# Optimization experiments

Measured on AMD Instinct MI355X. Metric: run time of the kernel, lower is better.

Reference implementation:

```python
import jax, jax.numpy as jnp
import numpy as np

B, T, I, H = 64, 512, 1024, 1024


def setup_inputs() -> dict:
    key = jax.random.key(0)
    k1, k2, k3, k4 = jax.random.split(key, 4)
    scale_ih = (6.0 / (H + I)) ** 0.5  # xavier_uniform bound
    scale_hh = (6.0 / (H + H)) ** 0.5
    return {
        "x": jax.random.normal(k1, (B, T, I), dtype=jnp.float32),
        "h0": jax.random.normal(k2, (1, B, H), dtype=jnp.float32),
        "W_ih": jax.random.uniform(k3, (H, I), dtype=jnp.float32, minval=-scale_ih, maxval=scale_ih),
        "b_ih": jnp.zeros((H,), dtype=jnp.float32),
        "W_hh": jax.random.uniform(k4, (H, H), dtype=jnp.float32, minval=-scale_hh, maxval=scale_hh),
        "b_hh": jnp.zeros((H,), dtype=jnp.float32),
    }


def reference(x, h0, W_ih, b_ih, W_hh, b_hh):
    # h_t = tanh(x_t @ W_ih^T + b_ih + h_{t-1} @ W_hh^T + b_hh)
    # Precompute the input projection for all timesteps (same math, batched GEMM).
    xp = jnp.einsum("bti,hi->tbh", x, W_ih) + b_ih  # [T,B,H]
    h = h0[0]  # [B,H]

    def step(h, xp_t):
        h_new = jnp.tanh(xp_t + h @ W_hh.T + b_hh)
        return h_new, h_new

    _, ys = jax.lax.scan(step, h, xp)  # ys: [T,B,H]
    return jnp.transpose(ys, (1, 0, 2))  # [B,T,H]
```

## Files before the change

kernel.cpp:

```cpp
#include <hip/hip_runtime.h>
#include <hip/hip_bf16.h>

#define BB_   64
#define TT_   512
#define II_   1024
#define HH_   1024

typedef _Float16 half8  __attribute__((ext_vector_type(8)));
typedef _Float16 half4v __attribute__((ext_vector_type(4)));
typedef float    f32x4  __attribute__((ext_vector_type(4)));

__device__ __forceinline__ float fast_tanh(float x) {
    float t = fminf(fmaxf(x, -16.f), 16.f);
    float e = __builtin_amdgcn_exp2f(t * 2.885390082f);
    return 1.f - 2.f * __builtin_amdgcn_rcpf(e + 1.f);
}

__global__ __launch_bounds__(256) void gemm_xp(const float* __restrict__ x,
                                               const float* __restrict__ Wih,
                                               const float* __restrict__ bih,
                                               float* __restrict__ out) {
    __shared__ alignas(16) _Float16 As[128 * 40];
    __shared__ alignas(16) _Float16 Bs[128 * 40];

    const int tid  = threadIdx.x;
    const int bm   = blockIdx.x >> 3;
    const int bn   = blockIdx.x & 7;
    const int M0   = bm * 128, N0 = bn * 128;
    const int lane = tid & 63, w = tid >> 6;
    const int wm   = (w & 1) * 64, wn = (w >> 1) * 64;
    const int ro   = lane & 15, q = lane >> 4;
    const int sr   = tid >> 3, sc = tid & 7;

    const f32x4 zero4 = {0.f, 0.f, 0.f, 0.f};
    f32x4 acc[4][4];
    #pragma unroll
    for (int i = 0; i < 4; ++i)
        #pragma unroll
        for (int j = 0; j < 4; ++j) acc[i][j] = zero4;

    for (int kk = 0; kk < 32; ++kk) {
        const int k0 = kk * 32;
        #pragma unroll
        for (int ir = 0; ir < 4; ++ir) {
            const int row = ir * 32 + sr;
            const float4 av = *(const float4*)(x   + (size_t)(M0 + row) * II_ + k0 + sc * 4);
            const float4 bv = *(const float4*)(Wih + (size_t)(N0 + row) * II_ + k0 + sc * 4);
            half4v ah = { (_Float16)av.x, (_Float16)av.y, (_Float16)av.z, (_Float16)av.w };
            half4v bh = { (_Float16)bv.x, (_Float16)bv.y, (_Float16)bv.z, (_Float16)bv.w };
            *(half4v*)(As + row * 40 + sc * 4) = ah;
            *(half4v*)(Bs + row * 40 + sc * 4) = bh;
        }
        __syncthreads();

        half8 a[4], b[4];
        #pragma unroll
        for (int i = 0; i < 4; ++i) {
            a[i] = *(const half8*)(As + (wm + i * 16 + ro) * 40 + q * 8);
            b[i] = *(const half8*)(Bs + (wn + i * 16 + ro) * 40 + q * 8);
        }
        #pragma unroll
        for (int i = 0; i < 4; ++i)
            #pragma unroll
            for (int j = 0; j < 4; ++j)
                acc[i][j] = __builtin_amdgcn_mfma_f32_16x16x32_f16(a[i], b[j], acc[i][j], 0, 0, 0);
        __syncthreads();
    }

    #pragma unroll
    for (int j = 0; j < 4; ++j) {
        const int col = N0 + wn + j * 16 + ro;
        const float bias = bih[col];
        #pragma unroll
        for (int i = 0; i < 4; ++i) {
            #pragma unroll
            for (int r = 0; r < 4; ++r) {
                const int rowg = M0 + wm + i * 16 + q * 4 + r;
                out[(size_t)rowg * HH_ + col] = acc[i][j][r] + bias;
            }
        }
    }
}

__global__ __launch_bounds__(256, 1) void rnn_steps(const float* __restrict__ Whh,
                                                    const float* __restrict__ bhh,
                                                    const float* __restrict__ h0,
                                                    float* __restrict__ out,
                                                    unsigned* __restrict__ comm) {
    __shared__ alignas(16) _Float16 hbuf[2][5][1032];

    const int tid  = threadIdx.x;
    const int lane = tid & 63;
    const int w    = tid >> 6;
    const int g    = blockIdx.x >> 4;
    const int wg   = blockIdx.x & 15;
    const int b0   = g * 4;
    const int j0   = wg * 64;
    const int ro   = lane & 15, q = lane >> 4;
    const int arow = (ro < 4) ? ro : 4;
    const int bat  = lane >> 4;
    const int colw = j0 + w * 16 + (lane & 15);

    half8 wf[4][8];
    {
        const float* wrow = Whh + (size_t)(j0 + w * 16 + ro) * HH_;
        #pragma unroll
        for (int kq = 0; kq < 4; ++kq) {
            #pragma unroll
            for (int ks = 0; ks < 8; ++ks) {
                const int kc = kq * 256 + ks * 32 + q * 8;
                const float4 w0 = *(const float4*)(wrow + kc);
                const float4 w1 = *(const float4*)(wrow + kc + 4);
                half8 hv;
                hv[0] = (_Float16)w0.x; hv[1] = (_Float16)w0.y;
                hv[2] = (_Float16)w0.z; hv[3] = (_Float16)w0.w;
                hv[4] = (_Float16)w1.x; hv[5] = (_Float16)w1.y;
                hv[6] = (_Float16)w1.z; hv[7] = (_Float16)w1.w;
                wf[kq][ks] = hv;
            }
        }
    }
    const float bhh_r = bhh[colw];

    for (int i = tid; i < 1032; i += 256) {
        hbuf[0][4][i] = (_Float16)0.f;
        hbuf[1][4][i] = (_Float16)0.f;
    }

    const f32x4 zero4 = {0.f, 0.f, 0.f, 0.f};

    #define TAGOK_(v) ((((unsigned)((v) >> 16) & 0xffffu) == su) & \
                       ((unsigned)((v) >> 48) == su))

    for (int s = 0; s < TT_; ++s) {
        const int slot = s & 1;

        const float xpv = out[((size_t)(b0 + bat) * TT_ + s) * HH_ + colw];

        unsigned* dstw = (unsigned*)(&hbuf[slot][w][0]);
        if (s == 0) {
            const float2* hrow = (const float2*)(h0 + (size_t)(b0 + w) * HH_);
            #pragma unroll
            for (int c = 0; c < 8; ++c) {
                const float2 hv = hrow[c * 64 + lane];
                union { _Float16 h[2]; unsigned u; } pk;
                pk.h[0] = (_Float16)hv.x; pk.h[1] = (_Float16)hv.y;
                dstw[c * 64 + lane] = pk.u;
            }
        } else {
            const unsigned su = (unsigned)s;
            const unsigned long long* sp = (const unsigned long long*)
                (comm + (size_t)slot * (BB_ * HH_) + (size_t)(b0 + w) * HH_);
            unsigned long long v0, v1, v2, v3, v4, v5, v6, v7;
            bool ok = false;
            while (!ok) {
                v0 = __hip_atomic_load(sp + 0 * 64 + lane, __ATOMIC_RELAXED, __HIP_MEMORY_SCOPE_AGENT);
                v1 = __hip_atomic_load(sp + 1 * 64 + lane, __ATOMIC_RELAXED, __HIP_MEMORY_SCOPE_AGENT);
                v2 = __hip_atomic_load(sp + 2 * 64 + lane, __ATOMIC_RELAXED, __HIP_MEMORY_SCOPE_AGENT);
                v3 = __hip_atomic_load(sp + 3 * 64 + lane, __ATOMIC_RELAXED, __HIP_MEMORY_SCOPE_AGENT);
                v4 = __hip_atomic_load(sp + 4 * 64 + lane, __ATOMIC_RELAXED, __HIP_MEMORY_SCOPE_AGENT);
                v5 = __hip_atomic_load(sp + 5 * 64 + lane, __ATOMIC_RELAXED, __HIP_MEMORY_SCOPE_AGENT);
                v6 = __hip_atomic_load(sp + 6 * 64 + lane, __ATOMIC_RELAXED, __HIP_MEMORY_SCOPE_AGENT);
                v7 = __hip_atomic_load(sp + 7 * 64 + lane, __ATOMIC_RELAXED, __HIP_MEMORY_SCOPE_AGENT);
                bool o = true;
                o &= TAGOK_(v0); o &= TAGOK_(v1); o &= TAGOK_(v2); o &= TAGOK_(v3);
                o &= TAGOK_(v4); o &= TAGOK_(v5); o &= TAGOK_(v6); o &= TAGOK_(v7);
                ok = o;
            }
            #define PACK_(x) ((unsigned)((x) & 0xffffull) | (((unsigned)((x) >> 32)) << 16))
            dstw[0 * 64 + lane] = PACK_(v0);
            dstw[1 * 64 + lane] = PACK_(v1);
            dstw[2 * 64 + lane] = PACK_(v2);
            dstw[3 * 64 + lane] = PACK_(v3);
            dstw[4 * 64 + lane] = PACK_(v4);
            dstw[5 * 64 + lane] = PACK_(v5);
            dstw[6 * 64 + lane] = PACK_(v6);
            dstw[7 * 64 + lane] = PACK_(v7);
            #undef PACK_
        }
        __syncthreads();

        f32x4 acc[4] = {zero4, zero4, zero4, zero4};
        const _Float16* abase = &hbuf[slot][0][0] + (size_t)arow * 1032;
        #pragma unroll
        for (int kq = 0; kq < 4; ++kq) {
            #pragma unroll
            for (int ks = 0; ks < 8; ++ks) {
                const half8 a = *(const half8*)(abase + kq * 256 + ks * 32 + q * 8);
                acc[kq] = __builtin_amdgcn_mfma_f32_16x16x32_f16(a, wf[kq][ks], acc[kq], 0, 0, 0);
            }
        }

        const f32x4 sum = acc[0] + acc[1] + acc[2] + acc[3];
        const float t0 = __shfl(sum[0], lane & 15);
        const float t1 = __shfl(sum[1], lane & 15);
        const float t2 = __shfl(sum[2], lane & 15);
        const float t3 = __shfl(sum[3], lane & 15);
        const float val = (bat == 0) ? t0 : (bat == 1) ? t1 : (bat == 2) ? t2 : t3;

        const float hnew = fast_tanh(xpv + bhh_r + val);

        union { _Float16 h; unsigned short us; } cv; cv.h = (_Float16)hnew;
        const unsigned word = ((unsigned)(s + 1) << 16) | (unsigned)cv.us;
        __hip_atomic_store(comm + (size_t)((s + 1) & 1) * (BB_ * HH_)
                                + (size_t)(b0 + bat) * HH_ + colw,
                           word, __ATOMIC_RELAXED, __HIP_MEMORY_SCOPE_AGENT);

        out[((size_t)(b0 + bat) * TT_ + s) * HH_ + colw] = hnew;
    }
    #undef TAGOK_
}

extern "C" void kernel_launch(void* const* d_in, const int* in_sizes, int n_in,
                              void* d_out, int out_size, void* d_ws, size_t ws_size,
                              hipStream_t stream) {
    (void)in_sizes; (void)n_in; (void)out_size; (void)ws_size;

    const float* x   = (const float*)d_in[0];
    const float* h0  = (const float*)d_in[1];
    const float* Wih = (const float*)d_in[2];
    const float* bih = (const float*)d_in[3];
    const float* Whh = (const float*)d_in[4];
    const float* bhh = (const float*)d_in[5];
    float* out = (float*)d_out;

    unsigned* comm = (unsigned*)d_ws;

    gemm_xp<<<2048, 256, 0, stream>>>(x, Wih, bih, out);
    rnn_steps<<<256, 256, 0, stream>>>(Whh, bhh, h0, out, comm);
}
```

Baseline: 1.543 ms.

## Double columns per wave in persistent RNN kernel, halve block count

Each wave now owns two 16-column tiles of W_hh held in registers (128 columns per block), and the persistent recurrent kernel launches 128 blocks instead of 256. Fewer blocks take part in each step's spin-wait exchange of the hidden state, and every hbuf A-fragment read is reused for two MFMAs. In exchange each wave holds twice the weight registers and issues twice the MFMA work per step, which lengthens the serial critical path.

```diff
diff --git a/kernel.cpp b/kernel.cpp
--- a/kernel.cpp
+++ b/kernel.cpp
@@ -92,18 +92,19 @@
     const int tid  = threadIdx.x;
     const int lane = tid & 63;
     const int w    = tid >> 6;
-    const int g    = blockIdx.x >> 4;
-    const int wg   = blockIdx.x & 15;
+    const int g    = blockIdx.x >> 3;
+    const int wg   = blockIdx.x & 7;
     const int b0   = g * 4;
-    const int j0   = wg * 64;
+    const int j0   = wg * 128;
     const int ro   = lane & 15, q = lane >> 4;
     const int arow = (ro < 4) ? ro : 4;
     const int bat  = lane >> 4;
-    const int colw = j0 + w * 16 + (lane & 15);
-
-    half8 wf[4][8];
-    {
-        const float* wrow = Whh + (size_t)(j0 + w * 16 + ro) * HH_;
+    const int cb   = j0 + w * 32;
+
+    half8 wf[2][4][8];
+    #pragma unroll
+    for (int t = 0; t < 2; ++t) {
+        const float* wrow = Whh + (size_t)(cb + t * 16 + ro) * HH_;
         #pragma unroll
         for (int kq = 0; kq < 4; ++kq) {
             #pragma unroll
@@ -116,11 +117,13 @@
                 hv[2] = (_Float16)w0.z; hv[3] = (_Float16)w0.w;
                 hv[4] = (_Float16)w1.x; hv[5] = (_Float16)w1.y;
                 hv[6] = (_Float16)w1.z; hv[7] = (_Float16)w1.w;
-                wf[kq][ks] = hv;
-            }
-        }
-    }
-    const float bhh_r = bhh[colw];
+                wf[t][kq][ks] = hv;
+            }
+        }
+    }
+    float bhh_r[2];
+    bhh_r[0] = bhh[cb + (lane & 15)];
+    bhh_r[1] = bhh[cb + 16 + (lane & 15)];
 
     for (int i = tid; i < 1032; i += 256) {
         hbuf[0][4][i] = (_Float16)0.f;
@@ -135,7 +138,9 @@
     for (int s = 0; s < TT_; ++s) {
         const int slot = s & 1;
 
-        const float xpv = out[((size_t)(b0 + bat) * TT_ + s) * HH_ + colw];
+        float xpv[2];
+        xpv[0] = out[((size_t)(b0 + bat) * TT_ + s) * HH_ + cb + (lane & 15)];
+        xpv[1] = out[((size_t)(b0 + bat) * TT_ + s) * HH_ + cb + 16 + (lane & 15)];
 
         unsigned* dstw = (unsigned*)(&hbuf[slot][w][0]);
         if (s == 0) {
@@ -180,33 +185,44 @@
         }
         __syncthreads();
 
-        f32x4 acc[4] = {zero4, zero4, zero4, zero4};
+        f32x4 acc[2][4] = {{zero4, zero4, zero4, zero4},
+                           {zero4, zero4, zero4, zero4}};
         const _Float16* abase = &hbuf[slot][0][0] + (size_t)arow * 1032;
         #pragma unroll
         for (int kq = 0; kq < 4; ++kq) {
             #pragma unroll
             for (int ks = 0; ks < 8; ++ks) {
                 const half8 a = *(const half8*)(abase + kq * 256 + ks * 32 + q * 8);
-                acc[kq] = __builtin_amdgcn_mfma_f32_16x16x32_f16(a, wf[kq][ks], acc[kq], 0, 0, 0);
-            }
-        }
-
-        const f32x4 sum = acc[0] + acc[1] + acc[2] + acc[3];
-        const float t0 = __shfl(sum[0], lane & 15);
-        const float t1 = __shfl(sum[1], lane & 15);
-        const float t2 = __shfl(sum[2], lane & 15);
-        const float t3 = __shfl(sum[3], lane & 15);
-        const float val = (bat == 0) ? t0 : (bat == 1) ? t1 : (bat == 2) ? t2 : t3;
-
-        const float hnew = fast_tanh(xpv + bhh_r + val);
-
-        union { _Float16 h; unsigned short us; } cv; cv.h = (_Float16)hnew;
-        const unsigned word = ((unsigned)(s + 1) << 16) | (unsigned)cv.us;
-        __hip_atomic_store(comm + (size_t)((s + 1) & 1) * (BB_ * HH_)
-                                + (size_t)(b0 + bat) * HH_ + colw,
-                           word, __ATOMIC_RELAXED, __HIP_MEMORY_SCOPE_AGENT);
-
-        out[((size_t)(b0 + bat) * TT_ + s) * HH_ + colw] = hnew;
+                acc[0][kq] = __builtin_amdgcn_mfma_f32_16x16x32_f16(a, wf[0][kq][ks], acc[0][kq], 0, 0, 0);
+                acc[1][kq] = __builtin_amdgcn_mfma_f32_16x16x32_f16(a, wf[1][kq][ks], acc[1][kq], 0, 0, 0);
+            }
+        }
+
+        float hn[2];
+        #pragma unroll
+        for (int t = 0; t < 2; ++t) {
+            const f32x4 sum = acc[t][0] + acc[t][1] + acc[t][2] + acc[t][3];
+            const float t0 = __shfl(sum[0], lane & 15);
+            const float t1 = __shfl(sum[1], lane & 15);
+            const float t2 = __shfl(sum[2], lane & 15);
+            const float t3 = __shfl(sum[3], lane & 15);
+            const float val = (bat == 0) ? t0 : (bat == 1) ? t1 : (bat == 2) ? t2 : t3;
+            hn[t] = fast_tanh(xpv[t] + bhh_r[t] + val);
+        }
+
+        const unsigned tagn = (unsigned)(s + 1) << 16;
+        unsigned* cbase = comm + (size_t)((s + 1) & 1) * (BB_ * HH_)
+                               + (size_t)(b0 + bat) * HH_;
+        #pragma unroll
+        for (int t = 0; t < 2; ++t) {
+            union { _Float16 h; unsigned short us; } cv; cv.h = (_Float16)hn[t];
+            __hip_atomic_store(cbase + cb + t * 16 + (lane & 15),
+                               tagn | (unsigned)cv.us, __ATOMIC_RELAXED,
+                               __HIP_MEMORY_SCOPE_AGENT);
+        }
+        #pragma unroll
+        for (int t = 0; t < 2; ++t)
+            out[((size_t)(b0 + bat) * TT_ + s) * HH_ + cb + t * 16 + (lane & 15)] = hn[t];
     }
     #undef TAGOK_
 }
@@ -227,5 +243,5 @@
     unsigned* comm = (unsigned*)d_ws;
 
     gemm_xp<<<2048, 256, 0, stream>>>(x, Wih, bih, out);
-    rnn_steps<<<256, 256, 0, stream>>>(Whh, bhh, h0, out, comm);
-}
+    rnn_steps<<<128, 256, 0, stream>>>(Whh, bhh, h0, out, comm);
+}
```

After: 1.751 ms. 1.13x slower.

## Fuse input projection GEMM into the persistent recurrent kernel

Applied to the files above, without the earlier changes.

Removes the separate x·W_ih GEMM kernel and instead keeps W_ih fragments in registers in each recurrent block, computing the input projection for 4 timesteps at a time from x staged into LDS. This eliminates the write and reread of the projected activations through the output buffer and the separate launch. In exchange it greatly increases register use, reads x redundantly across column blocks, and adds projection MFMAs and x loads onto the latency-bound step loop.

```diff
diff --git a/kernel.cpp b/kernel.cpp
--- a/kernel.cpp
+++ b/kernel.cpp
@@ -16,78 +16,16 @@
     return 1.f - 2.f * __builtin_amdgcn_rcpf(e + 1.f);
 }
 
-__global__ __launch_bounds__(256) void gemm_xp(const float* __restrict__ x,
-                                               const float* __restrict__ Wih,
-                                               const float* __restrict__ bih,
-                                               float* __restrict__ out) {
-    __shared__ alignas(16) _Float16 As[128 * 40];
-    __shared__ alignas(16) _Float16 Bs[128 * 40];
-
-    const int tid  = threadIdx.x;
-    const int bm   = blockIdx.x >> 3;
-    const int bn   = blockIdx.x & 7;
-    const int M0   = bm * 128, N0 = bn * 128;
-    const int lane = tid & 63, w = tid >> 6;
-    const int wm   = (w & 1) * 64, wn = (w >> 1) * 64;
-    const int ro   = lane & 15, q = lane >> 4;
-    const int sr   = tid >> 3, sc = tid & 7;
-
-    const f32x4 zero4 = {0.f, 0.f, 0.f, 0.f};
-    f32x4 acc[4][4];
-    #pragma unroll
-    for (int i = 0; i < 4; ++i)
-        #pragma unroll
-        for (int j = 0; j < 4; ++j) acc[i][j] = zero4;
-
-    for (int kk = 0; kk < 32; ++kk) {
-        const int k0 = kk * 32;
-        #pragma unroll
-        for (int ir = 0; ir < 4; ++ir) {
-            const int row = ir * 32 + sr;
-            const float4 av = *(const float4*)(x   + (size_t)(M0 + row) * II_ + k0 + sc * 4);
-            const float4 bv = *(const float4*)(Wih + (size_t)(N0 + row) * II_ + k0 + sc * 4);
-            half4v ah = { (_Float16)av.x, (_Float16)av.y, (_Float16)av.z, (_Float16)av.w };
-            half4v bh = { (_Float16)bv.x, (_Float16)bv.y, (_Float16)bv.z, (_Float16)bv.w };
-            *(half4v*)(As + row * 40 + sc * 4) = ah;
-            *(half4v*)(Bs + row * 40 + sc * 4) = bh;
-        }
-        __syncthreads();
-
-        half8 a[4], b[4];
-        #pragma unroll
-        for (int i = 0; i < 4; ++i) {
-            a[i] = *(const half8*)(As + (wm + i * 16 + ro) * 40 + q * 8);
-            b[i] = *(const half8*)(Bs + (wn + i * 16 + ro) * 40 + q * 8);
-        }
-        #pragma unroll
-        for (int i = 0; i < 4; ++i)
-            #pragma unroll
-            for (int j = 0; j < 4; ++j)
-                acc[i][j] = __builtin_amdgcn_mfma_f32_16x16x32_f16(a[i], b[j], acc[i][j], 0, 0, 0);
-        __syncthreads();
-    }
-
-    #pragma unroll
-    for (int j = 0; j < 4; ++j) {
-        const int col = N0 + wn + j * 16 + ro;
-        const float bias = bih[col];
-        #pragma unroll
-        for (int i = 0; i < 4; ++i) {
-            #pragma unroll
-            for (int r = 0; r < 4; ++r) {
-                const int rowg = M0 + wm + i * 16 + q * 4 + r;
-                out[(size_t)rowg * HH_ + col] = acc[i][j][r] + bias;
-            }
-        }
-    }
-}
-
-__global__ __launch_bounds__(256, 1) void rnn_steps(const float* __restrict__ Whh,
+__global__ __launch_bounds__(256, 1) void rnn_steps(const float* __restrict__ x,
+                                                    const float* __restrict__ Wih,
+                                                    const float* __restrict__ bih,
+                                                    const float* __restrict__ Whh,
                                                     const float* __restrict__ bhh,
                                                     const float* __restrict__ h0,
                                                     float* __restrict__ out,
                                                     unsigned* __restrict__ comm) {
     __shared__ alignas(16) _Float16 hbuf[2][5][1032];
+    __shared__ alignas(16) _Float16 xbuf[16][1032];
 
     const int tid  = threadIdx.x;
     const int lane = tid & 63;
@@ -101,9 +39,10 @@
     const int bat  = lane >> 4;
     const int colw = j0 + w * 16 + (lane & 15);
 
-    half8 wf[4][8];
+    half8 wf[4][8], wih_f[4][8];
     {
         const float* wrow = Whh + (size_t)(j0 + w * 16 + ro) * HH_;
+        const float* vrow = Wih + (size_t)(j0 + w * 16 + ro) * II_;
         #pragma unroll
         for (int kq = 0; kq < 4; ++kq) {
             #pragma unroll
@@ -117,96 +56,143 @@
                 hv[4] = (_Float16)w1.x; hv[5] = (_Float16)w1.y;
                 hv[6] = (_Float16)w1.z; hv[7] = (_Float16)w1.w;
                 wf[kq][ks] = hv;
+                const float4 u0 = *(const float4*)(vrow + kc);
+                const float4 u1 = *(const float4*)(vrow + kc + 4);
+                half8 gv;
+                gv[0] = (_Float16)u0.x; gv[1] = (_Float16)u0.y;
+                gv[2] = (_Float16)u0.z; gv[3] = (_Float16)u0.w;
+                gv[4] = (_Float16)u1.x; gv[5] = (_Float16)u1.y;
+                gv[6] = (_Float16)u1.z; gv[7] = (_Float16)u1.w;
+                wih_f[kq][ks] = gv;
             }
         }
     }
     const float bhh_r = bhh[colw];
+    const float bih_r = bih[colw];
 
     for (int i = tid; i < 1032; i += 256) {
         hbuf[0][4][i] = (_Float16)0.f;
         hbuf[1][4][i] = (_Float16)0.f;
     }
 
+    const int xrow = tid >> 4;
+    const int xseg = tid & 15;
+    const int xb   = xrow >> 2, xdt = xrow & 3;
+
     const f32x4 zero4 = {0.f, 0.f, 0.f, 0.f};
 
     #define TAGOK_(v) ((((unsigned)((v) >> 16) & 0xffffu) == su) & \
                        ((unsigned)((v) >> 48) == su))
 
-    for (int s = 0; s < TT_; ++s) {
-        const int slot = s & 1;
-
-        const float xpv = out[((size_t)(b0 + bat) * TT_ + s) * HH_ + colw];
-
-        unsigned* dstw = (unsigned*)(&hbuf[slot][w][0]);
-        if (s == 0) {
-            const float2* hrow = (const float2*)(h0 + (size_t)(b0 + w) * HH_);
+    f32x4 hold = zero4;
+
+    for (int sblk = 0; sblk < TT_ / 4; ++sblk) {
+        const float* xsrc = x + ((size_t)(b0 + xb) * TT_ + sblk * 4 + xdt) * II_;
+        float4 xl[16];
+        #pragma unroll
+        for (int i = 0; i < 16; ++i)
+            xl[i] = *(const float4*)(xsrc + xseg * 4 + i * 64);
+
+        #pragma unroll
+        for (int dt = 0; dt < 4; ++dt) {
+            const int s = sblk * 4 + dt;
+            const int slot = s & 1;
+
+            unsigned* dstw = (unsigned*)(&hbuf[slot][w][0]);
+            if (s == 0) {
+                const float2* hrow = (const float2*)(h0 + (size_t)(b0 + w) * HH_);
+                #pragma unroll
+                for (int c = 0; c < 8; ++c) {
+                    const float2 hv = hrow[c * 64 + lane];
+                    union { _Float16 h[2]; unsigned u; } pk;
+                    pk.h[0] = (_Float16)hv.x; pk.h[1] = (_Float16)hv.y;
+                    dstw[c * 64 + lane] = pk.u;
+                }
+            } else {
+                const unsigned su = (unsigned)s;
+                const unsigned long long* sp = (const unsigned long long*)
+                    (comm + (size_t)slot * (BB_ * HH_) + (size_t)(b0 + w) * HH_);
+                unsigned long long v0, v1, v2, v3, v4, v5, v6, v7;
+                bool ok = false;
+                while (!ok) {
+                    v0 = __hip_atomic_load(sp + 0 * 64 + lane, __ATOMIC_RELAXED, __HIP_MEMORY_SCOPE_AGENT);
+                    v1 = __hip_atomic_load(sp + 1 * 64 + lane, __ATOMIC_RELAXED, __HIP_MEMORY_SCOPE_AGENT);
+                    v2 = __hip_atomic_load(sp + 2 * 64 + lane, __ATOMIC_RELAXED, __HIP_MEMORY_SCOPE_AGENT);
+                    v3 = __hip_atomic_load(sp + 3 * 64 + lane, __ATOMIC_RELAXED, __HIP_MEMORY_SCOPE_AGENT);
+                    v4 = __hip_atomic_load(sp + 4 * 64 + lane, __ATOMIC_RELAXED, __HIP_MEMORY_SCOPE_AGENT);
+                    v5 = __hip_atomic_load(sp + 5 * 64 + lane, __ATOMIC_RELAXED, __HIP_MEMORY_SCOPE_AGENT);
+                    v6 = __hip_atomic_load(sp + 6 * 64 + lane, __ATOMIC_RELAXED, __HIP_MEMORY_SCOPE_AGENT);
+                    v7 = __hip_atomic_load(sp + 7 * 64 + lane, __ATOMIC_RELAXED, __HIP_MEMORY_SCOPE_AGENT);
+                    bool o = true;
+                    o &= TAGOK_(v0); o &= TAGOK_(v1); o &= TAGOK_(v2); o &= TAGOK_(v3);
+                    o &= TAGOK_(v4); o &= TAGOK_(v5); o &= TAGOK_(v6); o &= TAGOK_(v7);
+                    ok = o;
+                }
+                #define PACK_(x) ((unsigned)((x) & 0xffffull) | (((unsigned)((x) >> 32)) << 16))
+                dstw[0 * 64 + lane] = PACK_(v0);
+                dstw[1 * 64 + lane] = PACK_(v1);
+                dstw[2 * 64 + lane] = PACK_(v2);
+                dstw[3 * 64 + lane] = PACK_(v3);
+                dstw[4 * 64 + lane] = PACK_(v4);
+                dstw[5 * 64 + lane] = PACK_(v5);
+                dstw[6 * 64 + lane] = PACK_(v6);
+                dstw[7 * 64 + lane] = PACK_(v7);
+                #undef PACK_
+            }
+
+            if (dt == 0) {
+                #pragma unroll
+                for (int i = 0; i < 16; ++i) {
+                    half4v hx = { (_Float16)xl[i].x, (_Float16)xl[i].y,
+                                  (_Float16)xl[i].z, (_Float16)xl[i].w };
+                    *(half4v*)(&xbuf[xrow][xseg * 4 + i * 64]) = hx;
+                }
+            }
+            __syncthreads();
+
+            if (dt == 0) {
+                f32x4 accx[4] = {zero4, zero4, zero4, zero4};
+                const _Float16* xbase = &xbuf[0][0] + (size_t)ro * 1032;
+                #pragma unroll
+                for (int kq = 0; kq < 4; ++kq) {
+                    #pragma unroll
+                    for (int ks = 0; ks < 8; ++ks) {
+                        const half8 a = *(const half8*)(xbase + kq * 256 + ks * 32 + q * 8);
+                        accx[kq] = __builtin_amdgcn_mfma_f32_16x16x32_f16(a, wih_f[kq][ks], accx[kq], 0, 0, 0);
+                    }
+                }
+                hold = accx[0] + accx[1] + accx[2] + accx[3];
+                hold += (f32x4){bih_r, bih_r, bih_r, bih_r};
+            }
+
+            f32x4 acc[4] = {zero4, zero4, zero4, zero4};
+            const _Float16* abase = &hbuf[slot][0][0] + (size_t)arow * 1032;
             #pragma unroll
-            for (int c = 0; c < 8; ++c) {
-                const float2 hv = hrow[c * 64 + lane];
-                union { _Float16 h[2]; unsigned u; } pk;
-                pk.h[0] = (_Float16)hv.x; pk.h[1] = (_Float16)hv.y;
-                dstw[c * 64 + lane] = pk.u;
-            }
-        } else {
-            const unsigned su = (unsigned)s;
-            const unsigned long long* sp = (const unsigned long long*)
-                (comm + (size_t)slot * (BB_ * HH_) + (size_t)(b0 + w) * HH_);
-            unsigned long long v0, v1, v2, v3, v4, v5, v6, v7;
-            bool ok = false;
-            while (!ok) {
-                v0 = __hip_atomic_load(sp + 0 * 64 + lane, __ATOMIC_RELAXED, __HIP_MEMORY_SCOPE_AGENT);
-                v1 = __hip_atomic_load(sp + 1 * 64 + lane, __ATOMIC_RELAXED, __HIP_MEMORY_SCOPE_AGENT);
-                v2 = __hip_atomic_load(sp + 2 * 64 + lane, __ATOMIC_RELAXED, __HIP_MEMORY_SCOPE_AGENT);
-                v3 = __hip_atomic_load(sp + 3 * 64 + lane, __ATOMIC_RELAXED, __HIP_MEMORY_SCOPE_AGENT);
-                v4 = __hip_atomic_load(sp + 4 * 64 + lane, __ATOMIC_RELAXED, __HIP_MEMORY_SCOPE_AGENT);
-                v5 = __hip_atomic_load(sp + 5 * 64 + lane, __ATOMIC_RELAXED, __HIP_MEMORY_SCOPE_AGENT);
-                v6 = __hip_atomic_load(sp + 6 * 64 + lane, __ATOMIC_RELAXED, __HIP_MEMORY_SCOPE_AGENT);
-                v7 = __hip_atomic_load(sp + 7 * 64 + lane, __ATOMIC_RELAXED, __HIP_MEMORY_SCOPE_AGENT);
-                bool o = true;
-                o &= TAGOK_(v0); o &= TAGOK_(v1); o &= TAGOK_(v2); o &= TAGOK_(v3);
-                o &= TAGOK_(v4); o &= TAGOK_(v5); o &= TAGOK_(v6); o &= TAGOK_(v7);
-                ok = o;
-            }
-            #define PACK_(x) ((unsigned)((x) & 0xffffull) | (((unsigned)((x) >> 32)) << 16))
-            dstw[0 * 64 + lane] = PACK_(v0);
-            dstw[1 * 64 + lane] = PACK_(v1);
-            dstw[2 * 64 + lane] = PACK_(v2);
-            dstw[3 * 64 + lane] = PACK_(v3);
-            dstw[4 * 64 + lane] = PACK_(v4);
-            dstw[5 * 64 + lane] = PACK_(v5);
-            dstw[6 * 64 + lane] = PACK_(v6);
-            dstw[7 * 64 + lane] = PACK_(v7);
-            #undef PACK_
+            for (int kq = 0; kq < 4; ++kq) {
+                #pragma unroll
+                for (int ks = 0; ks < 8; ++ks) {
+                    const half8 a = *(const half8*)(abase + kq * 256 + ks * 32 + q * 8);
+                    acc[kq] = __builtin_amdgcn_mfma_f32_16x16x32_f16(a, wf[kq][ks], acc[kq], 0, 0, 0);
+                }
+            }
+
+            const f32x4 sum = acc[0] + acc[1] + acc[2] + acc[3];
+            const float t0 = __shfl(sum[0], lane & 15);
+            const float t1 = __shfl(sum[1], lane & 15);
+            const float t2 = __shfl(sum[2], lane & 15);
+            const float t3 = __shfl(sum[3], lane & 15);
+            const float val = (bat == 0) ? t0 : (bat == 1) ? t1 : (bat == 2) ? t2 : t3;
+
+            const float hnew = fast_tanh(hold[dt] + bhh_r + val);
+
+            union { _Float16 h; unsigned short us; } cv; cv.h = (_Float16)hnew;
+            const unsigned word = ((unsigned)(s + 1) << 16) | (unsigned)cv.us;
+            __hip_atomic_store(comm + (size_t)((s + 1) & 1) * (BB_ * HH_)
+                                    + (size_t)(b0 + bat) * HH_ + colw,
+                               word, __ATOMIC_RELAXED, __HIP_MEMORY_SCOPE_AGENT);
+
+            out[((size_t)(b0 + bat) * TT_ + s) * HH_ + colw] = hnew;
         }
-        __syncthreads();
-
-        f32x4 acc[4] = {zero4, zero4, zero4, zero4};
-        const _Float16* abase = &hbuf[slot][0][0] + (size_t)arow * 1032;
-        #pragma unroll
-        for (int kq = 0; kq < 4; ++kq) {
-            #pragma unroll
-            for (int ks = 0; ks < 8; ++ks) {
-                const half8 a = *(const half8*)(abase + kq * 256 + ks * 32 + q * 8);
-                acc[kq] = __builtin_amdgcn_mfma_f32_16x16x32_f16(a, wf[kq][ks], acc[kq], 0, 0, 0);
-            }
-        }
-
-        const f32x4 sum = acc[0] + acc[1] + acc[2] + acc[3];
-        const float t0 = __shfl(sum[0], lane & 15);
-        const float t1 = __shfl(sum[1], lane & 15);
-        const float t2 = __shfl(sum[2], lane & 15);
-        const float t3 = __shfl(sum[3], lane & 15);
-        const float val = (bat == 0) ? t0 : (bat == 1) ? t1 : (bat == 2) ? t2 : t3;
-
-        const float hnew = fast_tanh(xpv + bhh_r + val);
-
-        union { _Float16 h; unsigned short us; } cv; cv.h = (_Float16)hnew;
-        const unsigned word = ((unsigned)(s + 1) << 16) | (unsigned)cv.us;
-        __hip_atomic_store(comm + (size_t)((s + 1) & 1) * (BB_ * HH_)
-                                + (size_t)(b0 + bat) * HH_ + colw,
-                           word, __ATOMIC_RELAXED, __HIP_MEMORY_SCOPE_AGENT);
-
-        out[((size_t)(b0 + bat) * TT_ + s) * HH_ + colw] = hnew;
     }
     #undef TAGOK_
 }
@@ -226,6 +212,5 @@
 
     unsigned* comm = (unsigned*)d_ws;
 
-    gemm_xp<<<2048, 256, 0, stream>>>(x, Wih, bih, out);
-    rnn_steps<<<256, 256, 0, stream>>>(Whh, bhh, h0, out, comm);
+    rnn_steps<<<256, 256, 0, stream>>>(x, Wih, bih, Whh, bhh, h0, out, comm);
 }
```

Result: slower. 1.866 ms (+20.9%).
